# Performance work log

Measured on AMD Instinct MI355X. Metric: run time of the kernel, lower is better.

## Reference

```python
import jax, jax.numpy as jnp
import numpy as np

D = 512
B = 8
N = 4096  # h = w = 64 grid


def _rmsnorm(x, eps=1e-6):
    # SimpleRMSNorm (no learned scale)
    return x * jax.lax.rsqrt(jnp.mean(jnp.square(x), axis=-1, keepdims=True) + eps)


def setup_inputs() -> dict:
    key = jax.random.key(0)
    ks = jax.random.split(key, 8)
    s = 1.0 / np.sqrt(D)
    return {
        "x": jax.random.normal(ks[0], (B, N, D), jnp.float32),
        "lower_bound": jax.random.uniform(ks[1], (1,), jnp.float32),
        "W_in": jax.random.normal(ks[2], (D, D), jnp.float32) * s,
        "b_in": jnp.zeros((D,), jnp.float32),
        "W_f": jax.random.normal(ks[3], (D, D), jnp.float32) * s,
        "b_f": jnp.zeros((D,), jnp.float32),
        "theta": jax.random.normal(ks[4], (D,), jnp.float32),
        "W_g": jax.random.normal(ks[5], (D, D), jnp.float32) * s,
        "b_g": jnp.zeros((D,), jnp.float32),
        "W_out": jax.random.normal(ks[6], (D, D), jnp.float32) * s,
        "b_out": jnp.zeros((D,), jnp.float32),
    }


def _gated_scan(decay, u, axis, reverse):
    # linear recurrence h_t = decay_t * h_{t-1} + u_t via associative scan
    def comb(e1, e2):
        a1, x1 = e1
        a2, x2 = e2
        return a1 * a2, a2 * x1 + x2
    _, y = jax.lax.associative_scan(comb, (decay, u), axis=axis, reverse=reverse)
    return y


def reference(x, lower_bound, W_in, b_in, W_f, b_f, theta, W_g, b_g, W_out, b_out):
    b, n, d = x.shape
    h = int(np.sqrt(n))
    w = n // h
    # b n d -> n b d -> h w b d
    xg = jnp.transpose(x, (1, 0, 2)).reshape(h, w, b, d)
    u = jax.nn.silu(xg @ W_in + b_in)              # candidate input
    f = jax.nn.sigmoid(xg @ W_f + b_f)             # forget gate
    lam = lower_bound + (1.0 - lower_bound) * f    # lower-bounded decay magnitude
    # complex decay lam * exp(i theta); complex input (1 - lam) * u
    decay = (lam * jnp.cos(theta) + 1j * (lam * jnp.sin(theta))).astype(jnp.complex64)
    inp = ((1.0 - lam) * u).astype(jnp.complex64)
    # bidirectional 2D scan: forward/backward over both grid axes (non-causal)
    hidden = jnp.zeros_like(u)
    for axis in (0, 1):
        for rev in (False, True):
            hidden = hidden + _gated_scan(decay, inp, axis, rev).real
    g = jax.nn.sigmoid(xg @ W_g + b_g)             # output gate
    y = (g * _rmsnorm(hidden)) @ W_out + b_out
    # h w b d -> n b d -> b n d
    return jnp.transpose(y.reshape(n, b, d), (1, 0, 2))
```

## Files before the change

kernel.cpp:

```cpp
#include <hip/hip_runtime.h>
#include <math.h>

#define DD 512
#define HG 64
#define M_ROWS 32768
#define ELEMS ((size_t)M_ROWS * DD)
#define LOG2E 1.44269504088896340736f

typedef __attribute__((ext_vector_type(8))) _Float16 f16x8;
typedef __attribute__((ext_vector_type(2))) _Float16 f16x2;
typedef __attribute__((ext_vector_type(4))) float f32x4;

__device__ __forceinline__ float fexp2_(float x) { return __builtin_amdgcn_exp2f(x); }
__device__ __forceinline__ float frcp_(float x)  { return __builtin_amdgcn_rcpf(x); }
__device__ __forceinline__ float fsig_(float v)  { return frcp_(1.0f + fexp2_(-v * LOG2E)); }

__global__ __launch_bounds__(256) void prep(
    const float* __restrict__ x, _Float16* __restrict__ x16,
    const float* __restrict__ W0, const float* __restrict__ W1,
    const float* __restrict__ W2, const float* __restrict__ W3,
    _Float16* __restrict__ WT)
{
    __shared__ float tile[64][65];
    if (blockIdx.x < 8192) {
        const size_t i = ((size_t)blockIdx.x * 256 + threadIdx.x) * 8;
        const float4 a = *(const float4*)&x[i];
        const float4 b = *(const float4*)&x[i + 4];
        f16x8 h;
        h[0] = (_Float16)a.x; h[1] = (_Float16)a.y;
        h[2] = (_Float16)a.z; h[3] = (_Float16)a.w;
        h[4] = (_Float16)b.x; h[5] = (_Float16)b.y;
        h[6] = (_Float16)b.z; h[7] = (_Float16)b.w;
        *(f16x8*)&x16[i] = h;
        return;
    }
    const int wb = blockIdx.x - 8192;
    const int z = wb >> 6;
    const int rem = wb & 63;
    const int n0 = (rem & 7) * 64, k0 = (rem >> 3) * 64;
    const float* W = (z == 0) ? W0 : (z == 1) ? W1 : (z == 2) ? W2 : W3;
    _Float16* dst = WT + (size_t)z * DD * DD;
    const int t = threadIdx.x;
    const int tr = t >> 6, tc = t & 63;
#pragma unroll
    for (int p = 0; p < 16; ++p)
        tile[p * 4 + tr][tc] = W[(size_t)(k0 + p * 4 + tr) * DD + n0 + tc];
    __syncthreads();
#pragma unroll
    for (int p = 0; p < 16; ++p) {
        const int nn = p * 4 + tr;
        dst[(size_t)(n0 + nn) * DD + k0 + tc] = (_Float16)tile[tc][nn];
    }
}

template <int MODE>
__global__ __launch_bounds__(512, 2) void gemm8p(
    const _Float16* __restrict__ A, const _Float16* __restrict__ WT,
    const float* __restrict__ b0, const float* __restrict__ b1,
    const float* __restrict__ b2, const float* __restrict__ lb_ptr,
    void* __restrict__ o0, void* __restrict__ o1, void* __restrict__ o2)
{
    __shared__ __align__(16) _Float16 As[4][256][32];
    __shared__ __align__(16) _Float16 Bs[4][256][32];

    const int NB = (MODE == 0) ? 6 : 2;
    const int lin = blockIdx.x;
    const int xcd = lin & 7;
    const int qq  = lin >> 3;
    const int n_idx = qq % NB;
    const int mq  = qq / NB;
    const int m0 = (xcd + 8 * mq) * 256;
    const int n0 = n_idx * 256;

    const int tid  = threadIdx.x;
    const int wv   = tid >> 6;
    const int lane = tid & 63;
    const int wm = wv >> 2, wn = wv & 3;
    const int lrow = lane & 15;
    const int lk   = lane >> 4;

    const int srow = wv * 32 + (lane >> 2);
    const int schk = ((lane & 3) ^ ((lane >> 3) & 3)) * 8;
    const _Float16* Ag = A  + (size_t)(m0 + srow) * DD + schk;
    const _Float16* Bg = WT + (size_t)(n0 + srow) * DD + schk;

    const int ksw = (lk ^ ((lrow >> 1) & 3)) * 8;

    f32x4 acc[8][4];
#pragma unroll
    for (int i = 0; i < 8; ++i)
#pragma unroll
        for (int j = 0; j < 4; ++j) acc[i][j] = (f32x4)(0.f);

#define STG(BUF_, KT_) do {                                                    \
    _Pragma("unroll")                                                          \
    for (int j_ = 0; j_ < 2; ++j_) {                                           \
        __builtin_amdgcn_global_load_lds(                                      \
            (const __attribute__((address_space(1))) void*)                    \
              (Ag + (size_t)(j_ * 16) * DD + (KT_) * 32),                      \
            (__attribute__((address_space(3))) void*)                          \
              &As[BUF_][wv * 32 + j_ * 16][0], 16, 0, 0);                      \
        __builtin_amdgcn_global_load_lds(                                      \
            (const __attribute__((address_space(1))) void*)                    \
              (Bg + (size_t)(j_ * 16) * DD + (KT_) * 32),                      \
            (__attribute__((address_space(3))) void*)                          \
              &Bs[BUF_][wv * 32 + j_ * 16][0], 16, 0, 0);                      \
    } } while (0)

#define LDF(FA_, FB_, BUF_) do {                                               \
    _Pragma("unroll")                                                          \
    for (int q_ = 0; q_ < 8; ++q_)                                             \
        FA_[q_] = *(const f16x8*)&As[BUF_][wm * 128 + q_ * 16 + lrow][ksw];    \
    _Pragma("unroll")                                                          \
    for (int n_ = 0; n_ < 4; ++n_)                                             \
        FB_[n_] = *(const f16x8*)&Bs[BUF_][wn * 64 + n_ * 16 + lrow][ksw];     \
    } while (0)

#define MM(FA_, FB_) do {                                                      \
    __builtin_amdgcn_s_setprio(1);                                             \
    _Pragma("unroll")                                                          \
    for (int q_ = 0; q_ < 8; ++q_)                                             \
    _Pragma("unroll")                                                          \
    for (int n_ = 0; n_ < 4; ++n_)                                             \
        acc[q_][n_] = __builtin_amdgcn_mfma_f32_16x16x32_f16(                  \
            FA_[q_], FB_[n_], acc[q_][n_], 0, 0, 0);                           \
    __builtin_amdgcn_s_setprio(0);                                             \
    } while (0)

#define BAR __builtin_amdgcn_s_barrier()
#define VM(N_) asm volatile("s_waitcnt vmcnt(" #N_ ")" ::: "memory")

    f16x8 FA0[8], FB0[4], FA1[8], FB1[4];

    STG(0, 0); STG(1, 1); STG(2, 2);
    VM(4); BAR;
    LDF(FA0, FB0, 0);

#pragma unroll
    for (int g = 0; g < 16; ++g) {
        if (g + 3 < 16) STG((g + 3) & 3, g + 3);
        if (g + 1 < 16) {
            if (g & 1) LDF(FA0, FB0, (g + 1) & 3);
            else       LDF(FA1, FB1, (g + 1) & 3);
        }
        if (g & 1) MM(FA1, FB1);
        else       MM(FA0, FB0);
        if (g < 13)      { VM(4); BAR; }
        else if (g < 15) { VM(0); BAR; }
    }

#undef STG
#undef LDF
#undef MM
#undef BAR
#undef VM

    if (MODE == 0) {
        const int seg = n_idx >> 1;
        const float lbv = lb_ptr[0];
        const float* bias = (seg == 0) ? b0 : (seg == 1) ? b1 : b2;
        _Float16* outp = (seg == 0) ? (_Float16*)o0
                       : (seg == 1) ? (_Float16*)o1 : (_Float16*)o2;
        const int cbase = (n_idx & 1) * 256 + wn * 64;
#pragma unroll
        for (int q = 0; q < 8; ++q) {
            const int row = m0 + wm * 128 + q * 16 + lk * 4;
#pragma unroll
            for (int n = 0; n < 4; ++n) {
                const int col = cbase + n * 16 + lrow;
                const float bcol = bias[col];
#pragma unroll
                for (int r = 0; r < 4; ++r) {
                    const float v = acc[q][n][r] + bcol;
                    float res;
                    if (seg == 0)      res = (1.0f - lbv) * frcp_(1.0f + fexp2_(v * LOG2E));
                    else if (seg == 1) res = v * fsig_(v);
                    else               res = fsig_(v);
                    outp[(size_t)(row + r) * DD + col] = (_Float16)res;
                }
            }
        }
    } else {
        float* outp = (float*)o0;
#pragma unroll
        for (int q = 0; q < 8; ++q) {
            const int row = m0 + wm * 128 + q * 16 + lk * 4;
#pragma unroll
            for (int n = 0; n < 4; ++n) {
                const int col = n0 + wn * 64 + n * 16 + lrow;
                const float bcol = b0[col];
#pragma unroll
                for (int r = 0; r < 4; ++r)
                    outp[(size_t)(row + r) * DD + col] = acc[q][n][r] + bcol;
            }
        }
    }
}

#define CH 4
#define CL 16

#define STEP(K, YR0, YI0, YR1, YI1) {                                      \
    const float dm0_ = (float)dmr[K][0], dm1_ = (float)dmr[K][1];          \
    const float lm0_ = 1.0f - dm0_, lm1_ = 1.0f - dm1_;                    \
    float nr_ = fmaf(lm0_, c0 * (YR0) - s0 * (YI0), dm0_ * (float)ur[K][0]); \
    YI0 = lm0_ * (c0 * (YI0) + s0 * (YR0)); YR0 = nr_;                     \
    nr_ = fmaf(lm1_, c1 * (YR1) - s1 * (YI1), dm1_ * (float)ur[K][1]);     \
    YI1 = lm1_ * (c1 * (YI1) + s1 * (YR1)); YR1 = nr_; }

__global__ __launch_bounds__(256, 4) void scan2(
    const _Float16* __restrict__ dm, const _Float16* __restrict__ u,
    const float* __restrict__ theta,
    _Float16* __restrict__ ha, _Float16* __restrict__ hb)
{
    __shared__ float ex[CH][64][13];

    const int blk  = blockIdx.x & 2047;
    const bool is_i = blockIdx.x >= 2048;
    const int tid   = threadIdx.x;
    const int chunk = tid >> 6;
    const int dpl   = tid & 63;
    const int dpg   = blk & 3;
    const int line  = blk >> 2;
    const int d0    = (dpg * 64 + dpl) * 2;

    size_t base, stride;
    _Float16* hout;
    if (!is_i) {
        base = (size_t)line * (HG * DD) + d0; stride = DD; hout = ha;
    } else {
        const int bb = line >> 6, j = line & 63;
        base = (size_t)bb * (HG * HG * DD) + (size_t)j * DD + d0;
        stride = (size_t)HG * DD; hout = hb;
    }
    const size_t cbase = base + (size_t)(chunk * CL) * stride;

    float s0, c0, s1, c1;
    sincosf(theta[d0], &s0, &c0);
    sincosf(theta[d0 + 1], &s1, &c1);

    f16x2 dmr[CL], ur[CL];
#pragma unroll
    for (int k = 0; k < CL; ++k) {
        dmr[k] = *(const f16x2*)&dm[cbase + (size_t)k * stride];
        ur[k]  = *(const f16x2*)&u [cbase + (size_t)k * stride];
    }

    float fr0 = 0.f, fi0 = 0.f, fr1 = 0.f, fi1 = 0.f;
    float P0 = 1.f, P1 = 1.f;
#pragma unroll
    for (int k = 0; k < CL; ++k) {
        const float dm0_ = (float)dmr[k][0], dm1_ = (float)dmr[k][1];
        const float lm0_ = 1.0f - dm0_, lm1_ = 1.0f - dm1_;
        P0 *= lm0_; P1 *= lm1_;
        float nr_ = fmaf(lm0_, c0 * fr0 - s0 * fi0, dm0_ * (float)ur[k][0]);
        fi0 = lm0_ * (c0 * fi0 + s0 * fr0); fr0 = nr_;
        nr_ = fmaf(lm1_, c1 * fr1 - s1 * fi1, dm1_ * (float)ur[k][1]);
        fi1 = lm1_ * (c1 * fi1 + s1 * fr1); fr1 = nr_;
    }
    float br0 = 0.f, bi0 = 0.f, br1 = 0.f, bi1 = 0.f;
#pragma unroll
    for (int k = CL - 1; k >= 0; --k) STEP(k, br0, bi0, br1, bi1);

    float rc0 = c0, rs0 = s0, rc1 = c1, rs1 = s1;
#pragma unroll
    for (int q = 0; q < 4; ++q) {
        float t0 = rc0 * rc0 - rs0 * rs0; rs0 = 2.f * rc0 * rs0; rc0 = t0;
        float t1 = rc1 * rc1 - rs1 * rs1; rs1 = 2.f * rc1 * rs1; rc1 = t1;
    }

    {
        float* e = ex[chunk][dpl];
        e[0]  = P0 * rc0; e[1]  = P0 * rs0;
        e[2]  = fr0;      e[3]  = fi0;
        e[4]  = br0;      e[5]  = bi0;
        e[6]  = P1 * rc1; e[7]  = P1 * rs1;
        e[8]  = fr1;      e[9]  = fi1;
        e[10] = br1;      e[11] = bi1;
    }
    __syncthreads();

    float cfr0 = 0.f, cfi0 = 0.f, cfr1 = 0.f, cfi1 = 0.f;
    for (int cc = 0; cc < chunk; ++cc) {
        const float* e = ex[cc][dpl];
        float nr = e[2] + e[0] * cfr0 - e[1] * cfi0;
        cfi0     = e[3] + e[0] * cfi0 + e[1] * cfr0;
        cfr0 = nr;
        nr       = e[8] + e[6] * cfr1 - e[7] * cfi1;
        cfi1     = e[9] + e[6] * cfi1 + e[7] * cfr1;
        cfr1 = nr;
    }
    float cbr0 = 0.f, cbi0 = 0.f, cbr1 = 0.f, cbi1 = 0.f;
    for (int cc = CH - 1; cc > chunk; --cc) {
        const float* e = ex[cc][dpl];
        float nr = e[4] + e[0] * cbr0 - e[1] * cbi0;
        cbi0     = e[5] + e[0] * cbi0 + e[1] * cbr0;
        cbr0 = nr;
        nr       = e[10] + e[6] * cbr1 - e[7] * cbi1;
        cbi1     = e[11] + e[6] * cbi1 + e[7] * cbr1;
        cbr1 = nr;
    }

    float yr0 = cfr0, yi0 = cfi0, yr1 = cfr1, yi1 = cfi1;
    f16x2 fres[CL];
#pragma unroll
    for (int k = 0; k < CL; ++k) {
        STEP(k, yr0, yi0, yr1, yi1);
        f16x2 p; p[0] = (_Float16)yr0; p[1] = (_Float16)yr1;
        fres[k] = p;
    }
    yr0 = cbr0; yi0 = cbi0; yr1 = cbr1; yi1 = cbi1;
#pragma unroll
    for (int k = CL - 1; k >= 0; --k) {
        STEP(k, yr0, yi0, yr1, yi1);
        f16x2 o;
        o[0] = (_Float16)((float)fres[k][0] + yr0);
        o[1] = (_Float16)((float)fres[k][1] + yr1);
        *(f16x2*)&hout[cbase + (size_t)k * stride] = o;
    }
}
#undef STEP

__global__ __launch_bounds__(256) void gate_rmsnorm(
    const _Float16* __restrict__ ha, const _Float16* __restrict__ hb,
    const _Float16* __restrict__ g, _Float16* __restrict__ v)
{
    const int row = blockIdx.x;
    const int t = threadIdx.x;
    const size_t b0 = (size_t)row * DD + t * 2;
    const f16x2 a = *(const f16x2*)&ha[b0];
    const f16x2 b = *(const f16x2*)&hb[b0];
    const float h0 = (float)a[0] + (float)b[0];
    const float h1 = (float)a[1] + (float)b[1];
    float ss = h0 * h0 + h1 * h1;
#pragma unroll
    for (int off = 32; off > 0; off >>= 1) ss += __shfl_down(ss, off, 64);
    __shared__ float wsum[4];
    __shared__ float rms_s;
    if ((t & 63) == 0) wsum[t >> 6] = ss;
    __syncthreads();
    if (t == 0) {
        const float tot = wsum[0] + wsum[1] + wsum[2] + wsum[3];
        rms_s = rsqrtf(tot * (1.0f / (float)DD) + 1e-6f);
    }
    __syncthreads();
    const float rms = rms_s;
    const f16x2 gg = *(const f16x2*)&g[b0];
    f16x2 o;
    o[0] = (_Float16)((float)gg[0] * h0 * rms);
    o[1] = (_Float16)((float)gg[1] * h1 * rms);
    *(f16x2*)&v[b0] = o;
}

extern "C" void kernel_launch(void* const* d_in, const int* in_sizes, int n_in,
                              void* d_out, int out_size, void* d_ws, size_t ws_size,
                              hipStream_t stream)
{
    const float* x     = (const float*)d_in[0];
    const float* lb    = (const float*)d_in[1];
    const float* W_in  = (const float*)d_in[2];
    const float* b_in  = (const float*)d_in[3];
    const float* W_f   = (const float*)d_in[4];
    const float* b_f   = (const float*)d_in[5];
    const float* theta = (const float*)d_in[6];
    const float* W_g   = (const float*)d_in[7];
    const float* b_g   = (const float*)d_in[8];
    const float* W_out = (const float*)d_in[9];
    const float* b_out = (const float*)d_in[10];

    float* out = (float*)d_out;
    char* wsb  = (char*)d_ws;

    _Float16* dm_v = (_Float16*)wsb;
    _Float16* u_b  = (_Float16*)(wsb + ELEMS * 2);
    _Float16* g_b  = (_Float16*)(wsb + ELEMS * 4);
    _Float16* WT   = (_Float16*)(wsb + ELEMS * 6);
    const size_t WSEG = (size_t)DD * DD;

    _Float16* ha  = (_Float16*)d_out;
    _Float16* x16 = (_Float16*)((char*)d_out + ELEMS * 2);
    _Float16* hb  = x16;

    prep<<<8448, 256, 0, stream>>>(x, x16, W_f, W_in, W_g, W_out, WT);

    gemm8p<0><<<768, 512, 0, stream>>>(x16, WT, b_f, b_in, b_g, lb,
                                       dm_v, u_b, g_b);

    scan2<<<4096, 256, 0, stream>>>(dm_v, u_b, theta, ha, hb);

    gate_rmsnorm<<<M_ROWS, 256, 0, stream>>>(ha, hb, g_b, dm_v);

    gemm8p<1><<<256, 512, 0, stream>>>(dm_v, WT + 3 * WSEG, b_out, nullptr,
                                       nullptr, nullptr, out, nullptr, nullptr);
}
```

Measured before the change: 286.0 us.

## Restructure GEMM main loop into fine-grained half-tile phases with barriers

Replaces the double-buffered fragment loop with a phased schedule. Each K-tile is split into two M-halves, and each phase loads a quarter of the fragments, issues part of the next global-to-LDS stage, waits on lgkmcnt, and runs 16 MFMAs between barriers. The aim is to cut register pressure from the two full fragment sets and to interleave LDS reads, async global loads and MFMA more evenly. The cost is many more barriers per tile and strict waitcnt points that could serialize the work.

Measured after the change: 286.9 us. About the same (+0.3%).

```diff
diff --git a/kernel.cpp b/kernel.cpp
--- a/kernel.cpp
+++ b/kernel.cpp
@@ -92,68 +92,103 @@
 #pragma unroll
         for (int j = 0; j < 4; ++j) acc[i][j] = (f32x4)(0.f);
 
-#define STG(BUF_, KT_) do {                                                    \
-    _Pragma("unroll")                                                          \
-    for (int j_ = 0; j_ < 2; ++j_) {                                           \
+    f16x8 fa[4], fb[2][4];
+
+#define STGA(J_) do {                                                          \
+    _Pragma("unroll")                                                          \
+    for (int j_ = 0; j_ < 2; ++j_)                                             \
         __builtin_amdgcn_global_load_lds(                                      \
             (const __attribute__((address_space(1))) void*)                    \
-              (Ag + (size_t)(j_ * 16) * DD + (KT_) * 32),                      \
+              (Ag + (size_t)(j_ * 16) * DD + (J_) * 32),                       \
             (__attribute__((address_space(3))) void*)                          \
-              &As[BUF_][wv * 32 + j_ * 16][0], 16, 0, 0);                      \
+              &As[(J_) & 3][wv * 32 + j_ * 16][0], 16, 0, 0);                  \
+    } while (0)
+
+#define STGB(J_) do {                                                          \
+    _Pragma("unroll")                                                          \
+    for (int j_ = 0; j_ < 2; ++j_)                                             \
         __builtin_amdgcn_global_load_lds(                                      \
             (const __attribute__((address_space(1))) void*)                    \
-              (Bg + (size_t)(j_ * 16) * DD + (KT_) * 32),                      \
+              (Bg + (size_t)(j_ * 16) * DD + (J_) * 32),                       \
             (__attribute__((address_space(3))) void*)                          \
-              &Bs[BUF_][wv * 32 + j_ * 16][0], 16, 0, 0);                      \
-    } } while (0)
-
-#define LDF(FA_, FB_, BUF_) do {                                               \
-    _Pragma("unroll")                                                          \
-    for (int q_ = 0; q_ < 8; ++q_)                                             \
-        FA_[q_] = *(const f16x8*)&As[BUF_][wm * 128 + q_ * 16 + lrow][ksw];    \
+              &Bs[(J_) & 3][wv * 32 + j_ * 16][0], 16, 0, 0);                  \
+    } while (0)
+
+#define LDFA(H_, BUF_) do {                                                    \
+    _Pragma("unroll")                                                          \
+    for (int q_ = 0; q_ < 4; ++q_)                                             \
+        fa[q_] = *(const f16x8*)                                               \
+            &As[BUF_][wm * 128 + (H_) * 64 + q_ * 16 + lrow][ksw];             \
+    } while (0)
+
+#define LDFB(KS_, BUF_) do {                                                   \
     _Pragma("unroll")                                                          \
     for (int n_ = 0; n_ < 4; ++n_)                                             \
-        FB_[n_] = *(const f16x8*)&Bs[BUF_][wn * 64 + n_ * 16 + lrow][ksw];     \
-    } while (0)
-
-#define MM(FA_, FB_) do {                                                      \
+        fb[KS_][n_] = *(const f16x8*)                                          \
+            &Bs[BUF_][wn * 64 + n_ * 16 + lrow][ksw];                          \
+    } while (0)
+
+#define MM16(H_, KS_) do {                                                     \
     __builtin_amdgcn_s_setprio(1);                                             \
     _Pragma("unroll")                                                          \
-    for (int q_ = 0; q_ < 8; ++q_)                                             \
+    for (int q_ = 0; q_ < 4; ++q_)                                             \
     _Pragma("unroll")                                                          \
     for (int n_ = 0; n_ < 4; ++n_)                                             \
-        acc[q_][n_] = __builtin_amdgcn_mfma_f32_16x16x32_f16(                  \
-            FA_[q_], FB_[n_], acc[q_][n_], 0, 0, 0);                           \
+        acc[(H_) * 4 + q_][n_] = __builtin_amdgcn_mfma_f32_16x16x32_f16(       \
+            fa[q_], fb[KS_][n_], acc[(H_) * 4 + q_][n_], 0, 0, 0);             \
     __builtin_amdgcn_s_setprio(0);                                             \
     } while (0)
 
-#define BAR __builtin_amdgcn_s_barrier()
+#define BAR   __builtin_amdgcn_s_barrier()
+#define LGKM0 do { asm volatile("s_waitcnt lgkmcnt(0)" ::: "memory");          \
+                   __builtin_amdgcn_sched_barrier(0); } while (0)
 #define VM(N_) asm volatile("s_waitcnt vmcnt(" #N_ ")" ::: "memory")
-
-    f16x8 FA0[8], FB0[4], FA1[8], FB1[4];
-
-    STG(0, 0); STG(1, 1); STG(2, 2);
-    VM(4); BAR;
-    LDF(FA0, FB0, 0);
-
-#pragma unroll
-    for (int g = 0; g < 16; ++g) {
-        if (g + 3 < 16) STG((g + 3) & 3, g + 3);
-        if (g + 1 < 16) {
-            if (g & 1) LDF(FA0, FB0, (g + 1) & 3);
-            else       LDF(FA1, FB1, (g + 1) & 3);
-        }
-        if (g & 1) MM(FA1, FB1);
-        else       MM(FA0, FB0);
-        if (g < 13)      { VM(4); BAR; }
-        else if (g < 15) { VM(0); BAR; }
-    }
-
-#undef STG
-#undef LDF
-#undef MM
+#define NOSYNC ((void)0)
+
+#define PHASE(LDS_, STG_, H_, KS_, TAIL_) do {                                 \
+    LDS_; STG_;                                                                \
+    BAR;                                                                       \
+    LGKM0;                                                                     \
+    MM16(H_, KS_);                                                             \
+    TAIL_;                                                                     \
+    BAR;                                                                       \
+    } while (0)
+
+    STGA(0); STGB(0); STGA(1); STGB(1); STGA(2); STGB(2);
+    VM(8); BAR;
+
+    PHASE({ LDFA(0, 0); LDFB(0, 0); }, STGA(3), 0, 0, NOSYNC);
+    PHASE(  LDFA(1, 0),               STGB(3), 1, 0, VM(8));
+    PHASE({ LDFA(0, 1); LDFB(1, 1); }, NOSYNC,  0, 1, NOSYNC);
+    PHASE(  LDFA(1, 1),               NOSYNC,  1, 1, VM(4));
+
+#pragma unroll
+    for (int T = 1; T < 7; ++T) {
+        const int bA = (2 * T) & 3, bB = (2 * T + 1) & 3;
+        const int jA = 2 * T + 2,   jB = 2 * T + 3;
+        PHASE({ LDFA(0, bA); LDFB(0, bA); }, STGA(jA), 0, 0, NOSYNC);
+        PHASE(  LDFA(1, bA),                STGB(jA), 1, 0, VM(4));
+        PHASE({ LDFA(0, bB); LDFB(1, bB); }, STGA(jB), 0, 1, NOSYNC);
+        PHASE(  LDFA(1, bB),                STGB(jB), 1, 1, VM(4));
+    }
+
+    PHASE({ LDFA(0, 2); LDFB(0, 2); }, NOSYNC, 0, 0, NOSYNC);
+    PHASE(  LDFA(1, 2),               NOSYNC, 1, 0, VM(0));
+    PHASE({ LDFA(0, 3); LDFB(1, 3); }, NOSYNC, 0, 1, NOSYNC);
+    LDFA(1, 3);
+    LGKM0;
+    MM16(1, 1);
+
+#undef STGA
+#undef STGB
+#undef LDFA
+#undef LDFB
+#undef MM16
 #undef BAR
+#undef LGKM0
 #undef VM
+#undef NOSYNC
+#undef PHASE
 
     if (MODE == 0) {
         const int seg = n_idx >> 1;
```
